# Performance work log

Hardware: AMD Instinct MI355X
Metric: run time of the kernel (lower is better)

Reference implementation:

```python
import jax, jax.numpy as jnp
import numpy as np

N_NODES = 100000
N_EDGES = 1600000
H_DIM = 64  # pos(32) + vel(32)


def _mlp_init(key, d_in, d_hid, d_out):
    k1, k2 = jax.random.split(key)
    s1 = 1.0 / np.sqrt(d_in)
    s2 = 1.0 / np.sqrt(d_hid)
    w1 = jax.random.uniform(k1, (d_in, d_hid), jnp.float32, -s1, s1)
    w2 = jax.random.uniform(k2, (d_hid, d_out), jnp.float32, -s2, s2)
    return w1, jnp.zeros((d_hid,), jnp.float32), w2, jnp.zeros((d_out,), jnp.float32)


def setup_inputs() -> dict:
    key = jax.random.key(0)
    ks = jax.random.split(key, 6)
    pos = jax.random.normal(ks[0], (N_NODES, 32), jnp.float32)
    vel = jax.random.normal(ks[1], (N_NODES, 32), jnp.float32)
    edge_index = jax.random.randint(ks[2], (2, N_EDGES), 0, N_NODES, jnp.int32)
    msg_w1, msg_b1, msg_w2, msg_b2 = _mlp_init(ks[3], 2 * H_DIM, 64, 64)
    upd_w1, upd_b1, upd_w2, upd_b2 = _mlp_init(ks[4], H_DIM + 64, 64, 64)
    sp = 1.0 / np.sqrt(64)
    pred_w = jax.random.uniform(ks[5], (64, 32), jnp.float32, -sp, sp)
    pred_b = jnp.zeros((32,), jnp.float32)
    return dict(pos=pos, vel=vel, edge_index=edge_index,
                msg_w1=msg_w1, msg_b1=msg_b1, msg_w2=msg_w2, msg_b2=msg_b2,
                upd_w1=upd_w1, upd_b1=upd_b1, upd_w2=upd_w2, upd_b2=upd_b2,
                pred_w=pred_w, pred_b=pred_b)


def reference(pos, vel, edge_index,
              msg_w1, msg_b1, msg_w2, msg_b2,
              upd_w1, upd_b1, upd_w2, upd_b2,
              pred_w, pred_b):
    n = pos.shape[0]
    h = jnp.concatenate([pos, vel], axis=-1)              # [N, 64]
    src, dst = edge_index[0], edge_index[1]
    h_i = h[dst]                                          # [E, 64] target nodes
    h_j = h[src]                                          # [E, 64] source nodes
    # message MLP on concat(h_i, h_j)
    m = jnp.concatenate([h_i, h_j], axis=-1)              # [E, 128]
    m = jax.nn.relu(m @ msg_w1 + msg_b1) @ msg_w2 + msg_b2  # [E, 64]
    # scatter-add aggregate to target nodes
    aggr = jax.ops.segment_sum(m, dst, num_segments=n)    # [N, 64]
    # update MLP on concat(h, aggr)
    u = jnp.concatenate([h, aggr], axis=-1)               # [N, 128]
    u = jax.nn.relu(u @ upd_w1 + upd_b1) @ upd_w2 + upd_b2  # [N, 64]
    # linear prediction head -> acceleration
    return u @ pred_w + pred_b                            # [N, 32]
```

## Files before the change

### kernel.cpp

```cpp
#include <hip/hip_runtime.h>

#define NN 100000
#define NE 1600000
#define SB   391
#define NBKT 391
#define EPB  4096

typedef _Float16 f16x8 __attribute__((ext_vector_type(8)));
typedef float    f32x4 __attribute__((ext_vector_type(4)));

#define ZB   1563
#define PHB  3125
#define PWB  13

extern "C" __global__ void __launch_bounds__(256)
prep_kernel(const float* __restrict__ pos, const float* __restrict__ vel,
            const int* __restrict__ ei,
            const float* __restrict__ mw1, const float* __restrict__ mw2,
            const float* __restrict__ uw1, const float* __restrict__ uw2,
            const float* __restrict__ pw,
            _Float16* __restrict__ hh,
            _Float16* __restrict__ mw1f, _Float16* __restrict__ mw2f,
            _Float16* __restrict__ uw1f, _Float16* __restrict__ uw2f,
            _Float16* __restrict__ pwf,
            float* __restrict__ aggr, int* __restrict__ cntm)
{
    __shared__ int lh[NBKT];
    const int b = blockIdx.x, tid = threadIdx.x;
    if (b < ZB) {
        float4* p = (float4*)aggr;
        const int base4 = b * 1024 + tid;
        const float4 z = make_float4(0.f, 0.f, 0.f, 0.f);
#pragma unroll
        for (int k = 0; k < 4; ++k) {
            const int idx = base4 + k * 256;
            if (idx < NN * 16) p[idx] = z;
        }
    } else if (b < ZB + PHB) {
        const int t = (b - ZB) * 256 + tid;
        const int node = t >> 3, seg = t & 7;
        const float* src = (seg < 4) ? pos + (size_t)node * 32 + seg * 8
                                     : vel + (size_t)node * 32 + (seg - 4) * 8;
        const float4 a = ((const float4*)src)[0];
        const float4 c = ((const float4*)src)[1];
        f16x8 r;
        r[0]=(_Float16)a.x; r[1]=(_Float16)a.y; r[2]=(_Float16)a.z; r[3]=(_Float16)a.w;
        r[4]=(_Float16)c.x; r[5]=(_Float16)c.y; r[6]=(_Float16)c.z; r[7]=(_Float16)c.w;
        *(f16x8*)(hh + (size_t)node * 64 + seg * 8) = r;
    } else if (b < ZB + PHB + PWB) {
        const int t2 = (b - ZB - PHB) * 256 + tid;
        if (t2 < 1024) {
            const int t = t2 >> 8, kk = (t2 >> 6) & 3, l = t2 & 63;
            f16x8 r;
#pragma unroll
            for (int j = 0; j < 8; ++j)
                r[j] = (_Float16)mw1[(kk * 32 + (l >> 4) * 8 + j) * 64 + t * 16 + (l & 15)];
            *(f16x8*)(mw1f + (size_t)t2 * 8) = r;
        } else if (t2 < 1536) {
            const int i = t2 - 1024;
            const int t = i >> 7, kk = (i >> 6) & 1, l = i & 63;
            f16x8 r;
#pragma unroll
            for (int j = 0; j < 8; ++j)
                r[j] = (_Float16)mw2[(kk * 32 + (l >> 4) * 8 + j) * 64 + t * 16 + (l & 15)];
            *(f16x8*)(mw2f + (size_t)i * 8) = r;
        } else if (t2 < 2560) {
            const int i = t2 - 1536;
            const int t = i >> 8, kk = (i >> 6) & 3, l = i & 63;
            f16x8 r;
#pragma unroll
            for (int j = 0; j < 8; ++j)
                r[j] = (_Float16)uw1[(kk * 32 + (l >> 4) * 8 + j) * 64 + t * 16 + (l & 15)];
            *(f16x8*)(uw1f + (size_t)i * 8) = r;
        } else if (t2 < 3072) {
            const int i = t2 - 2560;
            const int t = i >> 7, kk = (i >> 6) & 1, l = i & 63;
            f16x8 r;
#pragma unroll
            for (int j = 0; j < 8; ++j)
                r[j] = (_Float16)uw2[(kk * 32 + (l >> 4) * 8 + j) * 64 + t * 16 + (l & 15)];
            *(f16x8*)(uw2f + (size_t)i * 8) = r;
        } else if (t2 < 3328) {
            const int i = t2 - 3072;
            const int t = i >> 7, kk = (i >> 6) & 1, l = i & 63;
            f16x8 r;
#pragma unroll
            for (int j = 0; j < 8; ++j)
                r[j] = (_Float16)pw[(kk * 32 + (l >> 4) * 8 + j) * 32 + t * 16 + (l & 15)];
            *(f16x8*)(pwf + (size_t)i * 8) = r;
        }
    } else {
        const int blk = b - (ZB + PHB + PWB);
        for (int i = tid; i < NBKT; i += 256) lh[i] = 0;
        __syncthreads();
        const int e0 = blk * EPB;
#pragma unroll
        for (int k = 0; k < EPB / 256; ++k) {
            const int e = e0 + k * 256 + tid;
            if (e < NE) atomicAdd(&lh[ei[NE + e] >> 8], 1);
        }
        __syncthreads();
        for (int i = tid; i < NBKT; i += 256) cntm[blk * NBKT + i] = lh[i];
    }
}

extern "C" __global__ void __launch_bounds__(512)
scancol_kernel(const int* __restrict__ cntm, int* __restrict__ offs,
               int* __restrict__ btot)
{
    __shared__ int s[512];
    const int tid = threadIdx.x, bkt = blockIdx.x;
    const int v = (tid < SB) ? cntm[tid * NBKT + bkt] : 0;
    s[tid] = v;
    __syncthreads();
    for (int off = 1; off < 512; off <<= 1) {
        int t = (tid >= off) ? s[tid - off] : 0;
        __syncthreads();
        s[tid] += t;
        __syncthreads();
    }
    if (tid < SB) offs[tid * NBKT + bkt] = s[tid] - v;
    if (tid == SB - 1) btot[bkt] = s[tid];
}

extern "C" __global__ void __launch_bounds__(512)
scanb_kernel(const int* __restrict__ btot, int* __restrict__ bbase)
{
    __shared__ int s[512];
    const int tid = threadIdx.x;
    const int v = (tid < NBKT) ? btot[tid] : 0;
    s[tid] = v;
    __syncthreads();
    for (int off = 1; off < 512; off <<= 1) {
        int t = (tid >= off) ? s[tid - off] : 0;
        __syncthreads();
        s[tid] += t;
        __syncthreads();
    }
    if (tid < NBKT) bbase[tid] = s[tid] - v;
    if (tid == NBKT - 1) bbase[NBKT] = s[tid];
}

extern "C" __global__ void __launch_bounds__(256)
sortC_kernel(const int* __restrict__ ei, const int* __restrict__ offs,
             const int* __restrict__ bbase, int2* __restrict__ sd_tmp)
{
    __shared__ int lh[NBKT];
    __shared__ int lo[NBKT];
    const int tid = threadIdx.x, blk = blockIdx.x;
    for (int i = tid; i < NBKT; i += 256) {
        lh[i] = 0;
        lo[i] = bbase[i] + offs[blk * NBKT + i];
    }
    __syncthreads();
    const int e0 = blk * EPB;
#pragma unroll
    for (int k = 0; k < EPB / 256; ++k) {
        const int e = e0 + k * 256 + tid;
        if (e < NE) {
            const int s = ei[e], d = ei[NE + e];
            const int bkt = d >> 8;
            const int r = atomicAdd(&lh[bkt], 1);
            sd_tmp[lo[bkt] + r] = make_int2(s, d);
        }
    }
}

extern "C" __global__ void __launch_bounds__(256)
sortD_kernel(const int2* __restrict__ sd_tmp, const int* __restrict__ bbase,
             int2* __restrict__ sd2)
{
    __shared__ int h[256];
    __shared__ int s[256];
    __shared__ int dbase[256];
    const int tid = threadIdx.x, bkt = blockIdx.x;
    const int s0 = bbase[bkt], s1 = bbase[bkt + 1];
    const int n = s1 - s0;
    h[tid] = 0;
    __syncthreads();
    for (int k = tid; k < n; k += 256)
        atomicAdd(&h[sd_tmp[s0 + k].y & 255], 1);
    __syncthreads();
    const int v = h[tid];
    s[tid] = v;
    __syncthreads();
    for (int off = 1; off < 256; off <<= 1) {
        int t = (tid >= off) ? s[tid - off] : 0;
        __syncthreads();
        s[tid] += t;
        __syncthreads();
    }
    dbase[tid] = s[tid] - v;
    __syncthreads();
    h[tid] = 0;
    __syncthreads();
    for (int k = tid; k < n; k += 256) {
        const int2 e = sd_tmp[s0 + k];
        const int dl = e.y & 255;
        const int r = atomicAdd(&h[dl], 1);
        sd2[s0 + dbase[dl] + r] = e;
    }
}

extern "C" __global__ void __launch_bounds__(512, 4)
edgeagg_kernel(const _Float16* __restrict__ hh,
               const int2* __restrict__ sd,
               const _Float16* __restrict__ w1f, const _Float16* __restrict__ w2f,
               const float* __restrict__ b1, const float* __restrict__ b2,
               float* __restrict__ aggr)
{
    __shared__ _Float16 sW1[4 * 4 * 64 * 8];
    __shared__ _Float16 sW2[4 * 2 * 64 * 8];
    __shared__ _Float16 sT[8][16 * 64];

    const int tid = threadIdx.x;
    const int wave = tid >> 6, lane = tid & 63;
    const int m = lane & 15, g = lane >> 4;
    const int wslot = (blockIdx.x * 8 + wave) * 64;

    const int2 sdv = sd[wslot + lane];

    const int prevd = __shfl_up(sdv.y, 1, 64);
    const unsigned long long bmask = __ballot(lane == 0 || sdv.y != prevd);

    {
        const uint4* g1 = (const uint4*)w1f; uint4* s1 = (uint4*)sW1;
#pragma unroll
        for (int i = 0; i < 2; ++i) s1[i * 512 + tid] = g1[i * 512 + tid];
        const uint4* g2 = (const uint4*)w2f; uint4* s2 = (uint4*)sW2;
        s2[tid] = g2[tid];
    }

    const float bb1[4] = { b1[m], b1[16 + m], b1[32 + m], b1[48 + m] };
    const float bb2[4] = { b2[m], b2[16 + m], b2[32 + m], b2[48 + m] };

    __syncthreads();

    _Float16* Y = sT[wave];

    float racc = 0.0f;
    int   rnode = __builtin_amdgcn_readlane(sdv.y, 0);
    int   firstRun = 1;

    f16x8 Abuf[2][4];
    {
        const int ns = __shfl(sdv.x, m, 64);
        const int nd = __shfl(sdv.y, m, 64);
        const _Float16* hd = hh + (size_t)nd * 64 + g * 8;
        const _Float16* hs = hh + (size_t)ns * 64 + g * 8;
        Abuf[0][0] = *(const f16x8*)(hd);
        Abuf[0][1] = *(const f16x8*)(hd + 32);
        Abuf[0][2] = *(const f16x8*)(hs);
        Abuf[0][3] = *(const f16x8*)(hs + 32);
    }

#pragma unroll
    for (int it = 0; it < 4; ++it) {
        const int cur = it & 1;
        if (it < 3) {
            const int ns = __shfl(sdv.x, (it + 1) * 16 + m, 64);
            const int nd = __shfl(sdv.y, (it + 1) * 16 + m, 64);
            const _Float16* hd = hh + (size_t)nd * 64 + g * 8;
            const _Float16* hs = hh + (size_t)ns * 64 + g * 8;
            Abuf[cur ^ 1][0] = *(const f16x8*)(hd);
            Abuf[cur ^ 1][1] = *(const f16x8*)(hd + 32);
            Abuf[cur ^ 1][2] = *(const f16x8*)(hs);
            Abuf[cur ^ 1][3] = *(const f16x8*)(hs + 32);
        }

        f32x4 acc[4] = {};
#pragma unroll
        for (int t = 0; t < 4; ++t) {
#pragma unroll
            for (int kk = 0; kk < 4; ++kk) {
                const f16x8 b = *(const f16x8*)(sW1 + ((t * 4 + kk) * 64 + lane) * 8);
                acc[t] = __builtin_amdgcn_mfma_f32_16x16x32_f16(Abuf[cur][kk], b, acc[t], 0, 0, 0);
            }
        }

#pragma unroll
        for (int t = 0; t < 4; ++t) {
#pragma unroll
            for (int r = 0; r < 4; ++r) {
                const float y = fmaxf(acc[t][r] + bb1[t], 0.0f);
                const int row = g * 4 + r, col = t * 16 + m;
                const int byteoff = row * 128 + ((2 * col) ^ ((row & 7) << 4));
                *(_Float16*)((char*)Y + byteoff) = (_Float16)y;
            }
        }
        asm volatile("s_waitcnt lgkmcnt(0)" ::: "memory");
        __builtin_amdgcn_sched_barrier(0);

        f16x8 a2[2];
#pragma unroll
        for (int kk = 0; kk < 2; ++kk) {
            const int c = kk * 4 + g;
            a2[kk] = *(const f16x8*)((char*)Y + m * 128 + ((c * 16) ^ ((m & 7) << 4)));
        }
        asm volatile("s_waitcnt lgkmcnt(0)" ::: "memory");
        __builtin_amdgcn_sched_barrier(0);

        f32x4 acc2[4] = {};
#pragma unroll
        for (int kk = 0; kk < 2; ++kk) {
#pragma unroll
            for (int t = 0; t < 4; ++t) {
                const f16x8 b = *(const f16x8*)(sW2 + ((t * 2 + kk) * 64 + lane) * 8);
                acc2[t] = __builtin_amdgcn_mfma_f32_16x16x32_f16(a2[kk], b, acc2[t], 0, 0, 0);
            }
        }
#pragma unroll
        for (int t = 0; t < 4; ++t)
#pragma unroll
            for (int r = 0; r < 4; ++r) acc2[t][r] += bb2[t];

        const unsigned tm = (unsigned)((bmask >> (it * 16)) & 0xFFFFull) | 0x10000u;
        if (tm == 0x10000u) {
            float p0 = 0.f, p1 = 0.f, p2 = 0.f, p3 = 0.f;
#pragma unroll
            for (int r = 0; r < 4; ++r) {
                p0 += acc2[0][r]; p1 += acc2[1][r];
                p2 += acc2[2][r]; p3 += acc2[3][r];
            }
            p0 += __shfl_xor(p0, 16); p0 += __shfl_xor(p0, 32);
            p1 += __shfl_xor(p1, 16); p1 += __shfl_xor(p1, 32);
            p2 += __shfl_xor(p2, 16); p2 += __shfl_xor(p2, 32);
            p3 += __shfl_xor(p3, 16); p3 += __shfl_xor(p3, 32);
            racc += (g == 0) ? p0 : (g == 1) ? p1 : (g == 2) ? p2 : p3;
        } else {
            int a = 0;
            while (a < 16) {
                const int b = a + 1 + __builtin_ctz(tm >> (a + 1));
                const int d = __builtin_amdgcn_readlane(sdv.y, it * 16 + a);
                if (d != rnode) {
                    float* ap = aggr + (size_t)rnode * 64 + lane;
                    if (firstRun) atomicAdd(ap, racc);
                    else          *ap = racc;
                    firstRun = 0; racc = 0.0f; rnode = d;
                }
                float p0 = 0.f, p1 = 0.f, p2 = 0.f, p3 = 0.f;
#pragma unroll
                for (int r = 0; r < 4; ++r) {
                    const int rowl = 4 * g + r;
                    const bool in = (rowl >= a) && (rowl < b);
                    p0 += in ? acc2[0][r] : 0.f;
                    p1 += in ? acc2[1][r] : 0.f;
                    p2 += in ? acc2[2][r] : 0.f;
                    p3 += in ? acc2[3][r] : 0.f;
                }
                p0 += __shfl_xor(p0, 16); p0 += __shfl_xor(p0, 32);
                p1 += __shfl_xor(p1, 16); p1 += __shfl_xor(p1, 32);
                p2 += __shfl_xor(p2, 16); p2 += __shfl_xor(p2, 32);
                p3 += __shfl_xor(p3, 16); p3 += __shfl_xor(p3, 32);
                racc += (g == 0) ? p0 : (g == 1) ? p1 : (g == 2) ? p2 : p3;
                a = b;
            }
        }
    }
    atomicAdd(aggr + (size_t)rnode * 64 + lane, racc);
}

extern "C" __global__ void __launch_bounds__(256)
node_mfma_kernel(const _Float16* __restrict__ hh, const float* __restrict__ aggr,
                 const _Float16* __restrict__ uw1f, const _Float16* __restrict__ uw2f,
                 const _Float16* __restrict__ pwf,
                 const float* __restrict__ b1, const float* __restrict__ b2,
                 const float* __restrict__ pb, float* __restrict__ out)
{
    __shared__ _Float16 sU1[4 * 4 * 64 * 8];
    __shared__ _Float16 sU2[4 * 2 * 64 * 8];
    __shared__ _Float16 sPW[2 * 2 * 64 * 8];
    __shared__ _Float16 sT[4][16 * 64];

    const int tid = threadIdx.x;
    {
        const uint4* g1 = (const uint4*)uw1f; uint4* s1 = (uint4*)sU1;
#pragma unroll
        for (int i = 0; i < 4; ++i) s1[i * 256 + tid] = g1[i * 256 + tid];
        const uint4* g2 = (const uint4*)uw2f; uint4* s2 = (uint4*)sU2;
#pragma unroll
        for (int i = 0; i < 2; ++i) s2[i * 256 + tid] = g2[i * 256 + tid];
        const uint4* g3 = (const uint4*)pwf;  uint4* s3 = (uint4*)sPW;
        s3[tid] = g3[tid];
    }
    __syncthreads();

    const int wave = tid >> 6, lane = tid & 63;
    const int m = lane & 15, g = lane >> 4;
    const int nb = (blockIdx.x * 4 + wave) * 16;
    const int v = nb + m;
    const int vl = (v < NN) ? v : (NN - 1);

    const _Float16* hv = hh + (size_t)vl * 64 + g * 8;
    const f16x8 a0 = *(const f16x8*)(hv);
    const f16x8 a1 = *(const f16x8*)(hv + 32);
    const float* av = aggr + (size_t)vl * 64 + g * 8;
    const float4 x0 = *(const float4*)(av),      x1 = *(const float4*)(av + 4);
    const float4 y0 = *(const float4*)(av + 32), y1 = *(const float4*)(av + 36);
    f16x8 a2, a3;
    a2[0]=(_Float16)x0.x; a2[1]=(_Float16)x0.y; a2[2]=(_Float16)x0.z; a2[3]=(_Float16)x0.w;
    a2[4]=(_Float16)x1.x; a2[5]=(_Float16)x1.y; a2[6]=(_Float16)x1.z; a2[7]=(_Float16)x1.w;
    a3[0]=(_Float16)y0.x; a3[1]=(_Float16)y0.y; a3[2]=(_Float16)y0.z; a3[3]=(_Float16)y0.w;
    a3[4]=(_Float16)y1.x; a3[5]=(_Float16)y1.y; a3[6]=(_Float16)y1.z; a3[7]=(_Float16)y1.w;

    f32x4 acc[4] = {};
#pragma unroll
    for (int t = 0; t < 4; ++t) {
        acc[t] = __builtin_amdgcn_mfma_f32_16x16x32_f16(
            a0, *(const f16x8*)(sU1 + ((t * 4 + 0) * 64 + lane) * 8), acc[t], 0, 0, 0);
        acc[t] = __builtin_amdgcn_mfma_f32_16x16x32_f16(
            a1, *(const f16x8*)(sU1 + ((t * 4 + 1) * 64 + lane) * 8), acc[t], 0, 0, 0);
        acc[t] = __builtin_amdgcn_mfma_f32_16x16x32_f16(
            a2, *(const f16x8*)(sU1 + ((t * 4 + 2) * 64 + lane) * 8), acc[t], 0, 0, 0);
        acc[t] = __builtin_amdgcn_mfma_f32_16x16x32_f16(
            a3, *(const f16x8*)(sU1 + ((t * 4 + 3) * 64 + lane) * 8), acc[t], 0, 0, 0);
    }

    _Float16* Y = sT[wave];
#pragma unroll
    for (int t = 0; t < 4; ++t) {
        const float bb = b1[t * 16 + m];
#pragma unroll
        for (int r = 0; r < 4; ++r) {
            const float y = fmaxf(acc[t][r] + bb, 0.0f);
            const int row = g * 4 + r, col = t * 16 + m;
            const int byteoff = row * 128 + ((2 * col) ^ ((row & 7) << 4));
            *(_Float16*)((char*)Y + byteoff) = (_Float16)y;
        }
    }
    asm volatile("s_waitcnt lgkmcnt(0)" ::: "memory");
    __builtin_amdgcn_sched_barrier(0);

    f16x8 ay[2];
#pragma unroll
    for (int kk = 0; kk < 2; ++kk) {
        const int c = kk * 4 + g;
        ay[kk] = *(const f16x8*)((char*)Y + m * 128 + ((c * 16) ^ ((m & 7) << 4)));
    }
    asm volatile("s_waitcnt lgkmcnt(0)" ::: "memory");
    __builtin_amdgcn_sched_barrier(0);

    f32x4 acc2[4] = {};
#pragma unroll
    for (int kk = 0; kk < 2; ++kk) {
#pragma unroll
        for (int t = 0; t < 4; ++t) {
            const f16x8 b = *(const f16x8*)(sU2 + ((t * 2 + kk) * 64 + lane) * 8);
            acc2[t] = __builtin_amdgcn_mfma_f32_16x16x32_f16(ay[kk], b, acc2[t], 0, 0, 0);
        }
    }

#pragma unroll
    for (int t = 0; t < 4; ++t) {
        const float bb = b2[t * 16 + m];
#pragma unroll
        for (int r = 0; r < 4; ++r) {
            const float u = acc2[t][r] + bb;
            const int row = g * 4 + r, col = t * 16 + m;
            const int byteoff = row * 128 + ((2 * col) ^ ((row & 7) << 4));
            *(_Float16*)((char*)Y + byteoff) = (_Float16)u;
        }
    }
    asm volatile("s_waitcnt lgkmcnt(0)" ::: "memory");
    __builtin_amdgcn_sched_barrier(0);

    f16x8 au[2];
#pragma unroll
    for (int kk = 0; kk < 2; ++kk) {
        const int c = kk * 4 + g;
        au[kk] = *(const f16x8*)((char*)Y + m * 128 + ((c * 16) ^ ((m & 7) << 4)));
    }
    asm volatile("s_waitcnt lgkmcnt(0)" ::: "memory");
    __builtin_amdgcn_sched_barrier(0);

    f32x4 acc3[2] = {};
#pragma unroll
    for (int kk = 0; kk < 2; ++kk) {
#pragma unroll
        for (int t = 0; t < 2; ++t) {
            const f16x8 b = *(const f16x8*)(sPW + ((t * 2 + kk) * 64 + lane) * 8);
            acc3[t] = __builtin_amdgcn_mfma_f32_16x16x32_f16(au[kk], b, acc3[t], 0, 0, 0);
        }
    }

    float* F = (float*)Y;
#pragma unroll
    for (int t = 0; t < 2; ++t) {
        const float bb = pb[t * 16 + m];
#pragma unroll
        for (int r = 0; r < 4; ++r) {
            const int row = g * 4 + r, col = t * 16 + m;
            const int byteoff = row * 128 + ((4 * col) ^ ((row & 7) << 4));
            *(float*)((char*)F + byteoff) = acc3[t][r] + bb;
        }
    }
    asm volatile("s_waitcnt lgkmcnt(0)" ::: "memory");
    __builtin_amdgcn_sched_barrier(0);

    const int row = lane >> 2, q = lane & 3;
    const float4 o0 = *(const float4*)((char*)F + row * 128 + ((q * 16)       ^ ((row & 7) << 4)));
    const float4 o1 = *(const float4*)((char*)F + row * 128 + (((q + 4) * 16) ^ ((row & 7) << 4)));
    if (nb + row < NN) {
        float4* op = (float4*)(out + (size_t)(nb + row) * 32);
        op[q]     = o0;
        op[q + 4] = o1;
    }
}

extern "C" __global__ void __launch_bounds__(256)
edge_msg_kernel(const float* __restrict__ pos, const float* __restrict__ vel,
                const int* __restrict__ ei,
                const float* __restrict__ w1, const float* __restrict__ b1,
                const float* __restrict__ w2, const float* __restrict__ b2,
                float* __restrict__ aggr)
{
    const int e = blockIdx.x * 256 + threadIdx.x;
    if (e >= NE) return;
    const int ns = ei[e];
    const int nd = ei[NE + e];
    float y[64];
#pragma unroll
    for (int j = 0; j < 64; ++j) y[j] = b1[j];
    for (int part = 0; part < 4; ++part) {
        const int    node  = (part < 2) ? nd : ns;
        const float* basep = (part & 1) ? vel : pos;
        const float4* xp = reinterpret_cast<const float4*>(basep + (size_t)node * 32);
        const float*  wp = w1 + part * 32 * 64;
        for (int q = 0; q < 8; ++q) {
            const float4 xv = xp[q];
#pragma unroll
            for (int kk = 0; kk < 4; ++kk) {
                const float xs = (kk == 0) ? xv.x : (kk == 1) ? xv.y
                               : (kk == 2) ? xv.z : xv.w;
                const float* wr = wp + (q * 4 + kk) * 64;
#pragma unroll
                for (int j = 0; j < 64; ++j) y[j] = fmaf(xs, wr[j], y[j]);
            }
        }
    }
    float mm[64];
#pragma unroll
    for (int c = 0; c < 64; ++c) mm[c] = b2[c];
#pragma unroll
    for (int j = 0; j < 64; ++j) {
        const float yj = fmaxf(y[j], 0.0f);
        const float* wr = w2 + j * 64;
#pragma unroll
        for (int c = 0; c < 64; ++c) mm[c] = fmaf(yj, wr[c], mm[c]);
    }
    float* ap = aggr + (size_t)nd * 64;
#pragma unroll
    for (int c = 0; c < 64; ++c) atomicAdd(ap + c, mm[c]);
}

extern "C" __global__ void __launch_bounds__(256)
node_upd_kernel(const float* __restrict__ pos, const float* __restrict__ vel,
                const float* __restrict__ aggr,
                const float* __restrict__ w1, const float* __restrict__ b1,
                const float* __restrict__ w2, const float* __restrict__ b2,
                const float* __restrict__ pw, const float* __restrict__ pb,
                float* __restrict__ out)
{
    const int v = blockIdx.x * 256 + threadIdx.x;
    if (v >= NN) return;

    float y[64];
#pragma unroll
    for (int j = 0; j < 64; ++j) y[j] = b1[j];
    for (int part = 0; part < 4; ++part) {
        const float* basep = (part == 0) ? pos + (size_t)v * 32
                           : (part == 1) ? vel + (size_t)v * 32
                           : aggr + (size_t)v * 64 + (size_t)(part - 2) * 32;
        const float4* xp = reinterpret_cast<const float4*>(basep);
        const float*  wp = w1 + part * 32 * 64;
        for (int q = 0; q < 8; ++q) {
            const float4 xv = xp[q];
#pragma unroll
            for (int kk = 0; kk < 4; ++kk) {
                const float xs = (kk == 0) ? xv.x : (kk == 1) ? xv.y
                               : (kk == 2) ? xv.z : xv.w;
                const float* wr = wp + (q * 4 + kk) * 64;
#pragma unroll
                for (int j = 0; j < 64; ++j) y[j] = fmaf(xs, wr[j], y[j]);
            }
        }
    }

    float u[64];
#pragma unroll
    for (int c = 0; c < 64; ++c) u[c] = b2[c];
#pragma unroll
    for (int j = 0; j < 64; ++j) {
        const float yj = fmaxf(y[j], 0.0f);
        const float* wr = w2 + j * 64;
#pragma unroll
        for (int c = 0; c < 64; ++c) u[c] = fmaf(yj, wr[c], u[c]);
    }

    float o[32];
#pragma unroll
    for (int c = 0; c < 32; ++c) o[c] = pb[c];
#pragma unroll
    for (int j = 0; j < 64; ++j) {
        const float* wr = pw + j * 32;
#pragma unroll
        for (int c = 0; c < 32; ++c) o[c] = fmaf(u[j], wr[c], o[c]);
    }

    float4* op = reinterpret_cast<float4*>(out + (size_t)v * 32);
#pragma unroll
    for (int q = 0; q < 8; ++q)
        op[q] = make_float4(o[q * 4], o[q * 4 + 1], o[q * 4 + 2], o[q * 4 + 3]);
}

extern "C" void kernel_launch(void* const* d_in, const int* in_sizes, int n_in,
                              void* d_out, int out_size, void* d_ws, size_t ws_size,
                              hipStream_t stream)
{
    const float* pos = (const float*)d_in[0];
    const float* vel = (const float*)d_in[1];
    const int*   ei  = (const int*)d_in[2];
    const float* mw1 = (const float*)d_in[3];
    const float* mb1 = (const float*)d_in[4];
    const float* mw2 = (const float*)d_in[5];
    const float* mb2 = (const float*)d_in[6];
    const float* uw1 = (const float*)d_in[7];
    const float* ub1 = (const float*)d_in[8];
    const float* uw2 = (const float*)d_in[9];
    const float* ub2 = (const float*)d_in[10];
    const float* pw  = (const float*)d_in[11];
    const float* pb  = (const float*)d_in[12];
    float* out = (float*)d_out;

    char* ws = (char*)d_ws;
    size_t off = 0;
    float*    aggr   = (float*)(ws + off);    off += (size_t)NN * 64 * 4;
    _Float16* hh     = (_Float16*)(ws + off); off += (size_t)NN * 64 * 2;
    int2*     sd_tmp = (int2*)(ws + off);     off += (size_t)NE * 8;
    int2*     sd2    = (int2*)(ws + off);     off += (size_t)NE * 8;
    int*      cntm   = (int*)(ws + off);      off += (size_t)SB * NBKT * 4;
    int*      offs   = (int*)(ws + off);      off += (size_t)SB * NBKT * 4;
    int*      btot   = (int*)(ws + off);      off += 512 * 4;
    int*      bbase  = (int*)(ws + off);      off += 512 * 4;
    _Float16* mw1f   = (_Float16*)(ws + off); off += 1024 * 8 * 2;
    _Float16* mw2f   = (_Float16*)(ws + off); off += 512 * 8 * 2;
    _Float16* uw1f   = (_Float16*)(ws + off); off += 1024 * 8 * 2;
    _Float16* uw2f   = (_Float16*)(ws + off); off += 512 * 8 * 2;
    _Float16* pwf    = (_Float16*)(ws + off); off += 256 * 8 * 2;
    const size_t need_full = off;

    if (ws_size >= need_full) {
        prep_kernel<<<ZB + PHB + PWB + SB, 256, 0, stream>>>(
            pos, vel, ei, mw1, mw2, uw1, uw2, pw,
            hh, mw1f, mw2f, uw1f, uw2f, pwf, aggr, cntm);
        scancol_kernel<<<NBKT, 512, 0, stream>>>(cntm, offs, btot);
        scanb_kernel<<<1, 512, 0, stream>>>(btot, bbase);
        sortC_kernel<<<SB, 256, 0, stream>>>(ei, offs, bbase, sd_tmp);
        sortD_kernel<<<NBKT, 256, 0, stream>>>(sd_tmp, bbase, sd2);
        edgeagg_kernel<<<NE / 512, 512, 0, stream>>>(
            hh, sd2, mw1f, mw2f, mb1, mb2, aggr);
        node_mfma_kernel<<<(NN + 63) / 64, 256, 0, stream>>>(
            hh, aggr, uw1f, uw2f, pwf, ub1, ub2, pb, out);
    } else {
        float* aggr2 = (float*)d_ws;
        hipMemsetAsync(aggr2, 0, (size_t)NN * 64 * sizeof(float), stream);
        edge_msg_kernel<<<NE / 256, 256, 0, stream>>>(pos, vel, ei,
                                                      mw1, mb1, mw2, mb2, aggr2);
        node_upd_kernel<<<(NN + 255) / 256, 256, 0, stream>>>(
            pos, vel, aggr2, uw1, ub1, uw2, ub2, pw, pb, out);
    }
}
```

Baseline: 137.2 us.

## Use 32x32x16 MFMA in edge MLP and drop separate bucket-base scan kernel

The edge-aggregation kernel now uses 32x32x16 f16 MFMA tiles, handling 32 edges per pass instead of 16. The message weights are repacked to match, and the intermediate activation goes to a padded LDS tile instead of an XOR-swizzled one. Bucket base offsets are now taken with an atomicAdd on a global counter inside the column-scan kernel, which removes the single-block scanb launch. The buckets are then laid out in atomic arrival order rather than bucket order, so the sorted edge array is only grouped by destination, not globally sorted. The larger tiles raise register use, and the padded LDS tile may cause bank conflicts.

```diff
diff --git a/kernel.cpp b/kernel.cpp
--- a/kernel.cpp
+++ b/kernel.cpp
@@ -6,8 +6,9 @@
 #define NBKT 391
 #define EPB  4096
 
-typedef _Float16 f16x8 __attribute__((ext_vector_type(8)));
-typedef float    f32x4 __attribute__((ext_vector_type(4)));
+typedef _Float16 f16x8  __attribute__((ext_vector_type(8)));
+typedef float    f32x4  __attribute__((ext_vector_type(4)));
+typedef float    f32x16 __attribute__((ext_vector_type(16)));
 
 #define ZB   1563
 #define PHB  3125
@@ -50,19 +51,21 @@
     } else if (b < ZB + PHB + PWB) {
         const int t2 = (b - ZB - PHB) * 256 + tid;
         if (t2 < 1024) {
-            const int t = t2 >> 8, kk = (t2 >> 6) & 3, l = t2 & 63;
+            const int f = t2 >> 6, l = t2 & 63;
+            const int s = f >> 1, tt = f & 1;
             f16x8 r;
 #pragma unroll
             for (int j = 0; j < 8; ++j)
-                r[j] = (_Float16)mw1[(kk * 32 + (l >> 4) * 8 + j) * 64 + t * 16 + (l & 15)];
+                r[j] = (_Float16)mw1[(s * 16 + (l >> 5) * 8 + j) * 64 + tt * 32 + (l & 31)];
             *(f16x8*)(mw1f + (size_t)t2 * 8) = r;
         } else if (t2 < 1536) {
             const int i = t2 - 1024;
-            const int t = i >> 7, kk = (i >> 6) & 1, l = i & 63;
+            const int f2 = i >> 6, l = i & 63;
+            const int s2 = f2 >> 1, tt = f2 & 1;
             f16x8 r;
 #pragma unroll
             for (int j = 0; j < 8; ++j)
-                r[j] = (_Float16)mw2[(kk * 32 + (l >> 4) * 8 + j) * 64 + t * 16 + (l & 15)];
+                r[j] = (_Float16)mw2[(s2 * 16 + (l >> 5) * 8 + j) * 64 + tt * 32 + (l & 31)];
             *(f16x8*)(mw2f + (size_t)i * 8) = r;
         } else if (t2 < 2560) {
             const int i = t2 - 1536;
@@ -105,8 +108,9 @@
 }
 
 extern "C" __global__ void __launch_bounds__(512)
-scancol_kernel(const int* __restrict__ cntm, int* __restrict__ offs,
-               int* __restrict__ btot)
+scancol_kernel(const int* __restrict__ cntm, int* __restrict__ gtot,
+               int* __restrict__ offs, int* __restrict__ btot,
+               int* __restrict__ bbase)
 {
     __shared__ int s[512];
     const int tid = threadIdx.x, bkt = blockIdx.x;
@@ -120,25 +124,11 @@
         __syncthreads();
     }
     if (tid < SB) offs[tid * NBKT + bkt] = s[tid] - v;
-    if (tid == SB - 1) btot[bkt] = s[tid];
-}
-
-extern "C" __global__ void __launch_bounds__(512)
-scanb_kernel(const int* __restrict__ btot, int* __restrict__ bbase)
-{
-    __shared__ int s[512];
-    const int tid = threadIdx.x;
-    const int v = (tid < NBKT) ? btot[tid] : 0;
-    s[tid] = v;
-    __syncthreads();
-    for (int off = 1; off < 512; off <<= 1) {
-        int t = (tid >= off) ? s[tid - off] : 0;
-        __syncthreads();
-        s[tid] += t;
-        __syncthreads();
-    }
-    if (tid < NBKT) bbase[tid] = s[tid] - v;
-    if (tid == NBKT - 1) bbase[NBKT] = s[tid];
+    if (tid == SB - 1) {
+        const int tot = s[tid];
+        btot[bkt]  = tot;
+        bbase[bkt] = atomicAdd(gtot, tot);
+    }
 }
 
 extern "C" __global__ void __launch_bounds__(256)
@@ -168,14 +158,14 @@
 
 extern "C" __global__ void __launch_bounds__(256)
 sortD_kernel(const int2* __restrict__ sd_tmp, const int* __restrict__ bbase,
-             int2* __restrict__ sd2)
+             const int* __restrict__ btot, int2* __restrict__ sd2)
 {
     __shared__ int h[256];
     __shared__ int s[256];
     __shared__ int dbase[256];
     const int tid = threadIdx.x, bkt = blockIdx.x;
-    const int s0 = bbase[bkt], s1 = bbase[bkt + 1];
-    const int n = s1 - s0;
+    const int s0 = bbase[bkt];
+    const int n  = btot[bkt];
     h[tid] = 0;
     __syncthreads();
     for (int k = tid; k < n; k += 256)
@@ -209,150 +199,130 @@
                const float* __restrict__ b1, const float* __restrict__ b2,
                float* __restrict__ aggr)
 {
-    __shared__ _Float16 sW1[4 * 4 * 64 * 8];
-    __shared__ _Float16 sW2[4 * 2 * 64 * 8];
-    __shared__ _Float16 sT[8][16 * 64];
+    __shared__ _Float16 sW1[16 * 64 * 8];
+    __shared__ _Float16 sW2[8 * 64 * 8];
+    __shared__ _Float16 sY[8][32 * 68];
 
     const int tid = threadIdx.x;
     const int wave = tid >> 6, lane = tid & 63;
-    const int m = lane & 15, g = lane >> 4;
+    const int e32 = lane & 31, half = lane >> 5;
     const int wslot = (blockIdx.x * 8 + wave) * 64;
 
     const int2 sdv = sd[wslot + lane];
-
     const int prevd = __shfl_up(sdv.y, 1, 64);
     const unsigned long long bmask = __ballot(lane == 0 || sdv.y != prevd);
 
     {
         const uint4* g1 = (const uint4*)w1f; uint4* s1 = (uint4*)sW1;
-#pragma unroll
-        for (int i = 0; i < 2; ++i) s1[i * 512 + tid] = g1[i * 512 + tid];
+        s1[tid] = g1[tid]; s1[512 + tid] = g1[512 + tid];
         const uint4* g2 = (const uint4*)w2f; uint4* s2 = (uint4*)sW2;
         s2[tid] = g2[tid];
     }
 
-    const float bb1[4] = { b1[m], b1[16 + m], b1[32 + m], b1[48 + m] };
-    const float bb2[4] = { b2[m], b2[16 + m], b2[32 + m], b2[48 + m] };
-
-    __syncthreads();
-
-    _Float16* Y = sT[wave];
+    const float bb1_0 = b1[e32], bb1_1 = b1[32 + e32];
+    const float bb2_0 = b2[e32], bb2_1 = b2[32 + e32];
+
+    f16x8 A[8];
+    {
+        const int ns = __shfl(sdv.x, e32, 64);
+        const int nd = __shfl(sdv.y, e32, 64);
+        const _Float16* hd = hh + (size_t)nd * 64 + half * 8;
+        const _Float16* hs = hh + (size_t)ns * 64 + half * 8;
+        A[0] = *(const f16x8*)(hd);      A[1] = *(const f16x8*)(hd + 16);
+        A[2] = *(const f16x8*)(hd + 32); A[3] = *(const f16x8*)(hd + 48);
+        A[4] = *(const f16x8*)(hs);      A[5] = *(const f16x8*)(hs + 16);
+        A[6] = *(const f16x8*)(hs + 32); A[7] = *(const f16x8*)(hs + 48);
+    }
+    __syncthreads();
+
+    _Float16* Y = sY[wave];
 
     float racc = 0.0f;
     int   rnode = __builtin_amdgcn_readlane(sdv.y, 0);
     int   firstRun = 1;
 
-    f16x8 Abuf[2][4];
-    {
-        const int ns = __shfl(sdv.x, m, 64);
-        const int nd = __shfl(sdv.y, m, 64);
-        const _Float16* hd = hh + (size_t)nd * 64 + g * 8;
-        const _Float16* hs = hh + (size_t)ns * 64 + g * 8;
-        Abuf[0][0] = *(const f16x8*)(hd);
-        Abuf[0][1] = *(const f16x8*)(hd + 32);
-        Abuf[0][2] = *(const f16x8*)(hs);
-        Abuf[0][3] = *(const f16x8*)(hs + 32);
-    }
-
-#pragma unroll
-    for (int it = 0; it < 4; ++it) {
-        const int cur = it & 1;
-        if (it < 3) {
-            const int ns = __shfl(sdv.x, (it + 1) * 16 + m, 64);
-            const int nd = __shfl(sdv.y, (it + 1) * 16 + m, 64);
-            const _Float16* hd = hh + (size_t)nd * 64 + g * 8;
-            const _Float16* hs = hh + (size_t)ns * 64 + g * 8;
-            Abuf[cur ^ 1][0] = *(const f16x8*)(hd);
-            Abuf[cur ^ 1][1] = *(const f16x8*)(hd + 32);
-            Abuf[cur ^ 1][2] = *(const f16x8*)(hs);
-            Abuf[cur ^ 1][3] = *(const f16x8*)(hs + 32);
-        }
-
-        f32x4 acc[4] = {};
-#pragma unroll
-        for (int t = 0; t < 4; ++t) {
-#pragma unroll
-            for (int kk = 0; kk < 4; ++kk) {
-                const f16x8 b = *(const f16x8*)(sW1 + ((t * 4 + kk) * 64 + lane) * 8);
-                acc[t] = __builtin_amdgcn_mfma_f32_16x16x32_f16(Abuf[cur][kk], b, acc[t], 0, 0, 0);
-            }
-        }
-
-#pragma unroll
-        for (int t = 0; t < 4; ++t) {
-#pragma unroll
-            for (int r = 0; r < 4; ++r) {
-                const float y = fmaxf(acc[t][r] + bb1[t], 0.0f);
-                const int row = g * 4 + r, col = t * 16 + m;
-                const int byteoff = row * 128 + ((2 * col) ^ ((row & 7) << 4));
-                *(_Float16*)((char*)Y + byteoff) = (_Float16)y;
-            }
-        }
+#pragma unroll
+    for (int it = 0; it < 2; ++it) {
+        f32x16 acc0 = {}, acc1 = {};
+#pragma unroll
+        for (int s = 0; s < 8; ++s) {
+            const f16x8 b0 = *(const f16x8*)(sW1 + ((s * 2 + 0) * 64 + lane) * 8);
+            const f16x8 b1v = *(const f16x8*)(sW1 + ((s * 2 + 1) * 64 + lane) * 8);
+            acc0 = __builtin_amdgcn_mfma_f32_32x32x16_f16(A[s], b0, acc0, 0, 0, 0);
+            acc1 = __builtin_amdgcn_mfma_f32_32x32x16_f16(A[s], b1v, acc1, 0, 0, 0);
+        }
+
+#pragma unroll
+        for (int reg = 0; reg < 16; ++reg) {
+            const int row = (reg & 3) + 8 * (reg >> 2) + 4 * half;
+            _Float16* yr = Y + row * 68;
+            yr[e32]      = (_Float16)fmaxf(acc0[reg] + bb1_0, 0.0f);
+            yr[e32 + 32] = (_Float16)fmaxf(acc1[reg] + bb1_1, 0.0f);
+        }
+
+        if (it == 0) {
+            const int ns = __shfl(sdv.x, 32 + e32, 64);
+            const int nd = __shfl(sdv.y, 32 + e32, 64);
+            const _Float16* hd = hh + (size_t)nd * 64 + half * 8;
+            const _Float16* hs = hh + (size_t)ns * 64 + half * 8;
+            A[0] = *(const f16x8*)(hd);      A[1] = *(const f16x8*)(hd + 16);
+            A[2] = *(const f16x8*)(hd + 32); A[3] = *(const f16x8*)(hd + 48);
+            A[4] = *(const f16x8*)(hs);      A[5] = *(const f16x8*)(hs + 16);
+            A[6] = *(const f16x8*)(hs + 32); A[7] = *(const f16x8*)(hs + 48);
+        }
+
         asm volatile("s_waitcnt lgkmcnt(0)" ::: "memory");
         __builtin_amdgcn_sched_barrier(0);
 
-        f16x8 a2[2];
-#pragma unroll
-        for (int kk = 0; kk < 2; ++kk) {
-            const int c = kk * 4 + g;
-            a2[kk] = *(const f16x8*)((char*)Y + m * 128 + ((c * 16) ^ ((m & 7) << 4)));
-        }
+        f16x8 a2[4];
+#pragma unroll
+        for (int s2 = 0; s2 < 4; ++s2)
+            a2[s2] = *(const f16x8*)(Y + e32 * 68 + s2 * 16 + half * 8);
         asm volatile("s_waitcnt lgkmcnt(0)" ::: "memory");
         __builtin_amdgcn_sched_barrier(0);
 
-        f32x4 acc2[4] = {};
-#pragma unroll
-        for (int kk = 0; kk < 2; ++kk) {
-#pragma unroll
-            for (int t = 0; t < 4; ++t) {
-                const f16x8 b = *(const f16x8*)(sW2 + ((t * 2 + kk) * 64 + lane) * 8);
-                acc2[t] = __builtin_amdgcn_mfma_f32_16x16x32_f16(a2[kk], b, acc2[t], 0, 0, 0);
-            }
-        }
-#pragma unroll
-        for (int t = 0; t < 4; ++t)
-#pragma unroll
-            for (int r = 0; r < 4; ++r) acc2[t][r] += bb2[t];
-
-        const unsigned tm = (unsigned)((bmask >> (it * 16)) & 0xFFFFull) | 0x10000u;
-        if (tm == 0x10000u) {
-            float p0 = 0.f, p1 = 0.f, p2 = 0.f, p3 = 0.f;
-#pragma unroll
-            for (int r = 0; r < 4; ++r) {
-                p0 += acc2[0][r]; p1 += acc2[1][r];
-                p2 += acc2[2][r]; p3 += acc2[3][r];
-            }
-            p0 += __shfl_xor(p0, 16); p0 += __shfl_xor(p0, 32);
-            p1 += __shfl_xor(p1, 16); p1 += __shfl_xor(p1, 32);
-            p2 += __shfl_xor(p2, 16); p2 += __shfl_xor(p2, 32);
-            p3 += __shfl_xor(p3, 16); p3 += __shfl_xor(p3, 32);
-            racc += (g == 0) ? p0 : (g == 1) ? p1 : (g == 2) ? p2 : p3;
+        f32x16 m0 = {}, m1 = {};
+#pragma unroll
+        for (int s2 = 0; s2 < 4; ++s2) {
+            const f16x8 b0 = *(const f16x8*)(sW2 + ((s2 * 2 + 0) * 64 + lane) * 8);
+            const f16x8 b1v = *(const f16x8*)(sW2 + ((s2 * 2 + 1) * 64 + lane) * 8);
+            m0 = __builtin_amdgcn_mfma_f32_32x32x16_f16(a2[s2], b0, m0, 0, 0, 0);
+            m1 = __builtin_amdgcn_mfma_f32_32x32x16_f16(a2[s2], b1v, m1, 0, 0, 0);
+        }
+#pragma unroll
+        for (int reg = 0; reg < 16; ++reg) { m0[reg] += bb2_0; m1[reg] += bb2_1; }
+
+        const unsigned long long tm =
+            ((bmask >> (it * 32)) & 0xFFFFFFFFull) | (1ull << 32);
+        if (tm == (1ull << 32)) {
+            float p0 = 0.f, p1 = 0.f;
+#pragma unroll
+            for (int reg = 0; reg < 16; ++reg) { p0 += m0[reg]; p1 += m1[reg]; }
+            p0 += __shfl_xor(p0, 32);
+            p1 += __shfl_xor(p1, 32);
+            racc += half ? p1 : p0;
         } else {
             int a = 0;
-            while (a < 16) {
-                const int b = a + 1 + __builtin_ctz(tm >> (a + 1));
-                const int d = __builtin_amdgcn_readlane(sdv.y, it * 16 + a);
+            while (a < 32) {
+                const int b = a + 1 + __builtin_ctzll(tm >> (a + 1));
+                const int d = __builtin_amdgcn_readlane(sdv.y, it * 32 + a);
                 if (d != rnode) {
                     float* ap = aggr + (size_t)rnode * 64 + lane;
                     if (firstRun) atomicAdd(ap, racc);
                     else          *ap = racc;
                     firstRun = 0; racc = 0.0f; rnode = d;
                 }
-                float p0 = 0.f, p1 = 0.f, p2 = 0.f, p3 = 0.f;
-#pragma unroll
-                for (int r = 0; r < 4; ++r) {
-                    const int rowl = 4 * g + r;
-                    const bool in = (rowl >= a) && (rowl < b);
-                    p0 += in ? acc2[0][r] : 0.f;
-                    p1 += in ? acc2[1][r] : 0.f;
-                    p2 += in ? acc2[2][r] : 0.f;
-                    p3 += in ? acc2[3][r] : 0.f;
+                float p0 = 0.f, p1 = 0.f;
+#pragma unroll
+                for (int reg = 0; reg < 16; ++reg) {
+                    const int row = (reg & 3) + 8 * (reg >> 2) + 4 * half;
+                    const bool in = (row >= a) && (row < b);
+                    p0 += in ? m0[reg] : 0.f;
+                    p1 += in ? m1[reg] : 0.f;
                 }
-                p0 += __shfl_xor(p0, 16); p0 += __shfl_xor(p0, 32);
-                p1 += __shfl_xor(p1, 16); p1 += __shfl_xor(p1, 32);
-                p2 += __shfl_xor(p2, 16); p2 += __shfl_xor(p2, 32);
-                p3 += __shfl_xor(p3, 16); p3 += __shfl_xor(p3, 32);
-                racc += (g == 0) ? p0 : (g == 1) ? p1 : (g == 2) ? p2 : p3;
+                p0 += __shfl_xor(p0, 32);
+                p1 += __shfl_xor(p1, 32);
+                racc += half ? p1 : p0;
                 a = b;
             }
         }
@@ -642,6 +612,7 @@
     int*      offs   = (int*)(ws + off);      off += (size_t)SB * NBKT * 4;
     int*      btot   = (int*)(ws + off);      off += 512 * 4;
     int*      bbase  = (int*)(ws + off);      off += 512 * 4;
+    int*      gtot   = (int*)(ws + off);      off += 256;
     _Float16* mw1f   = (_Float16*)(ws + off); off += 1024 * 8 * 2;
     _Float16* mw2f   = (_Float16*)(ws + off); off += 512 * 8 * 2;
     _Float16* uw1f   = (_Float16*)(ws + off); off += 1024 * 8 * 2;
@@ -650,13 +621,13 @@
     const size_t need_full = off;
 
     if (ws_size >= need_full) {
+        hipMemsetAsync(gtot, 0, sizeof(int), stream);
         prep_kernel<<<ZB + PHB + PWB + SB, 256, 0, stream>>>(
             pos, vel, ei, mw1, mw2, uw1, uw2, pw,
             hh, mw1f, mw2f, uw1f, uw2f, pwf, aggr, cntm);
-        scancol_kernel<<<NBKT, 512, 0, stream>>>(cntm, offs, btot);
-        scanb_kernel<<<1, 512, 0, stream>>>(btot, bbase);
+        scancol_kernel<<<NBKT, 512, 0, stream>>>(cntm, gtot, offs, btot, bbase);
         sortC_kernel<<<SB, 256, 0, stream>>>(ei, offs, bbase, sd_tmp);
-        sortD_kernel<<<NBKT, 256, 0, stream>>>(sd_tmp, bbase, sd2);
+        sortD_kernel<<<NBKT, 256, 0, stream>>>(sd_tmp, bbase, btot, sd2);
         edgeagg_kernel<<<NE / 512, 512, 0, stream>>>(
             hh, sd2, mw1f, mw2f, mb1, mb2, aggr);
         node_mfma_kernel<<<(NN + 63) / 64, 256, 0, stream>>>(
```

After: 147.6 us. 1.08x slower.
